# Kernel optimization log

Hardware: AMD Instinct MI355X
Metric: run time of the kernel (lower is better)

Reference implementation:

```python
import jax, jax.numpy as jnp
import numpy as np

N_NODES = 100000
N_EDGES = 800000
IN_CH = 100
HID = 100   # 2 * out_channels
OUT = 50


def setup_inputs() -> dict:
    key = jax.random.key(0)
    ks = jax.random.split(key, 6)
    x = jax.random.normal(ks[0], (N_NODES, IN_CH), dtype=jnp.float32)
    edge_index = jax.random.randint(ks[1], (2, N_EDGES), 0, N_NODES, dtype=jnp.int32)
    # Glorot-ish init for the three GCN layer weights; zero biases.
    W1 = jax.random.normal(ks[2], (IN_CH, HID), dtype=jnp.float32) * (1.0 / np.sqrt(IN_CH))
    b1 = jnp.zeros((HID,), dtype=jnp.float32)
    W_mu = jax.random.normal(ks[3], (HID, OUT), dtype=jnp.float32) * (1.0 / np.sqrt(HID))
    b_mu = jnp.zeros((OUT,), dtype=jnp.float32)
    W_ls = jax.random.normal(ks[4], (HID, OUT), dtype=jnp.float32) * (1.0 / np.sqrt(HID))
    b_ls = jnp.zeros((OUT,), dtype=jnp.float32)
    return {"x": x, "edge_index": edge_index, "W1": W1, "b1": b1,
            "W_mu": W_mu, "b_mu": b_mu, "W_ls": W_ls, "b_ls": b_ls}


def _gcn_conv(x, W, b, src, dst, deg_inv_sqrt, n):
    # GCNConv: out = D^-1/2 (A + I) D^-1/2 (x W) + b
    h = x @ W                                      # transform first (smaller messages)
    norm = deg_inv_sqrt[src] * deg_inv_sqrt[dst]   # [E]
    agg = jax.ops.segment_sum(h[src] * norm[:, None], dst, num_segments=n)
    agg = agg + h * (deg_inv_sqrt * deg_inv_sqrt)[:, None]  # self-loop term
    return agg + b


def reference(x, edge_index, W1, b1, W_mu, b_mu, W_ls, b_ls):
    n = x.shape[0]
    src, dst = edge_index[0], edge_index[1]
    # degree with self-loops (GCN normalization, edge_weight = 1)
    deg = jax.ops.segment_sum(jnp.ones((edge_index.shape[1],), jnp.float32), dst,
                              num_segments=n) + 1.0
    deg_inv_sqrt = jax.lax.rsqrt(deg)
    h = jax.nn.relu(_gcn_conv(x, W1, b1, src, dst, deg_inv_sqrt, n))
    # dropout is identity in eval mode (p applied only during training)
    mu = _gcn_conv(h, W_mu, b_mu, src, dst, deg_inv_sqrt, n)
    logstd = _gcn_conv(h, W_ls, b_ls, src, dst, deg_inv_sqrt, n)
    return mu, logstd
```

## Files before the change

kernel.cpp:

```cpp
#include <hip/hip_runtime.h>

#define NN 100000
#define NE 800000
#define NBLK 196
#define BCAP 6144
#define EPB 8192
#define NPART ((NE + EPB - 1) / EPB)
#define PACKBLK 56

typedef unsigned short ushort_t;
typedef unsigned int uint_t;
typedef __attribute__((ext_vector_type(8))) short short8;
typedef __attribute__((ext_vector_type(4))) float floatx4;

__device__ __forceinline__ float bf2f(ushort_t u) {
    union { unsigned int i; float f; } v; v.i = ((unsigned int)u) << 16; return v.f;
}
__device__ __forceinline__ ushort_t f2bf(float f) {
    union { float f; unsigned int i; } v; v.f = f;
    unsigned int b = v.i + 0x7FFF + ((v.i >> 16) & 1);
    return (ushort_t)(b >> 16);
}
__device__ __forceinline__ uint_t pack2(float a, float b) {
    return (uint_t)f2bf(a) | ((uint_t)f2bf(b) << 16);
}

__global__ __launch_bounds__(256) void k_part(const int* __restrict__ src,
                                              const int* __restrict__ dst,
                                              int* __restrict__ bcnt,
                                              int* __restrict__ bedge,
                                              const float* __restrict__ W1,
                                              const float* __restrict__ Wmu,
                                              const float* __restrict__ Wls,
                                              uint_t* __restrict__ Wt1g,
                                              uint_t* __restrict__ Wt2g) {
    __shared__ int hist[NBLK];
    __shared__ int lbase[NBLK];
    const int blk = blockIdx.x, t = threadIdx.x;

    if (blk >= NPART) {
        int lidx = (blk - NPART) * 256 + t;
        int np = lidx >> 6;
        int kp = lidx & 63;
        int mat = np / 112, n = np - mat * 112;
        int k0 = kp * 2, k1 = k0 + 1;
        float w0 = 0.0f, w1 = 0.0f;
        if (mat == 0) {
            if (n < 100) {
                if (k0 < 100) w0 = W1[k0 * 100 + n];
                if (k1 < 100) w1 = W1[k1 * 100 + n];
            }
            Wt1g[n * 64 + kp] = pack2(w0, w1);
        } else {
            if (n < 50) {
                if (k0 < 100) w0 = Wmu[k0 * 50 + n];
                if (k1 < 100) w1 = Wmu[k1 * 50 + n];
            } else if (n < 100) {
                if (k0 < 100) w0 = Wls[k0 * 50 + (n - 50)];
                if (k1 < 100) w1 = Wls[k1 * 50 + (n - 50)];
            }
            Wt2g[n * 64 + kp] = pack2(w0, w1);
        }
        return;
    }

    const int e0 = blk * EPB;
    const int e1 = (e0 + EPB < NE) ? e0 + EPB : NE;

    if (t < NBLK) hist[t] = 0;
    __syncthreads();
    for (int e = e0 + t; e < e1; e += 256)
        atomicAdd(&hist[dst[e] >> 9], 1);
    __syncthreads();
    if (t < NBLK) {
        int h = hist[t];
        lbase[t] = (h > 0) ? atomicAdd(&bcnt[t], h) : 0;
    }
    __syncthreads();
    if (t < NBLK) hist[t] = lbase[t];
    __syncthreads();
    for (int e = e0 + t; e < e1; e += 256) {
        int d = dst[e];
        int b = d >> 9;
        int pos = atomicAdd(&hist[b], 1);
        bedge[b * BCAP + pos] = src[e] | ((d & 511) << 17);
    }
}

__global__ __launch_bounds__(256) void k_build(const int* __restrict__ bcnt,
                                               const int* __restrict__ bedge,
                                               float* __restrict__ dis,
                                               int* __restrict__ off,
                                               int* __restrict__ ssrc) {
    __shared__ int eb[BCAP];
    __shared__ int hist[512];
    __shared__ int sc[2][512];
    __shared__ int red[4];
    const int b = blockIdx.x, t = threadIdx.x;
    const int cnt = bcnt[b];
    const int* be = bedge + (size_t)b * BCAP;
    const int g0 = b * 512;

    hist[t] = 0; hist[t + 256] = 0;
    int part = (t < b) ? bcnt[t] : 0;
    #pragma unroll
    for (int o = 32; o > 0; o >>= 1) part += __shfl_down(part, o, 64);
    if ((t & 63) == 0) red[t >> 6] = part;
    __syncthreads();

    for (int i = t; i < cnt; i += 256) {
        int v = be[i];
        eb[i] = v;
        atomicAdd(&hist[v >> 17], 1);
    }
    __syncthreads();
    const int base0 = red[0] + red[1] + red[2] + red[3];

    sc[0][t] = hist[t];
    sc[0][t + 256] = hist[t + 256];
    __syncthreads();
    int c = 0;
    for (int o = 1; o < 512; o <<= 1) {
        int nxt = c ^ 1;
        #pragma unroll
        for (int q = 0; q < 2; ++q) {
            int j = t + q * 256;
            sc[nxt][j] = sc[c][j] + ((j >= o) ? sc[c][j - o] : 0);
        }
        c = nxt;
        __syncthreads();
    }

    #pragma unroll
    for (int q = 0; q < 2; ++q) {
        int j = t + q * 256, g = g0 + j;
        int o = base0 + ((j > 0) ? sc[c][j - 1] : 0);
        if (g < NN) dis[g] = rsqrtf((float)hist[j] + 1.0f);
        if (g <= NN) off[g] = o;
        hist[j] = o;
    }
    __syncthreads();

    for (int i = t; i < cnt; i += 256) {
        int v = eb[i];
        int pos = atomicAdd(&hist[v >> 17], 1);
        ssrc[pos] = v & 0x1FFFF;
    }
}

__global__ __launch_bounds__(256) void k_gemm1_mfma(
    const float* __restrict__ X, const uint_t* __restrict__ Wtg,
    const float* __restrict__ dis,
    ushort_t* __restrict__ H)
{
    __shared__ ushort_t Ws[112 * 136];
    const int tid = threadIdx.x;
    const int row0 = blockIdx.x * 64;

    for (int idx = tid; idx < 112 * 16; idx += 256) {
        int n = idx >> 4, c = idx & 15;
        uint4 v = *(const uint4*)&Wtg[n * 64 + c * 4];
        *(uint4*)&Ws[n * 136 + c * 8] = v;
    }
    __syncthreads();

    const int wave = tid >> 6, lane = tid & 63;
    const int quad = lane >> 4, l16 = lane & 15;
    int row = row0 + wave * 16 + l16;
    if (row >= NN) row = NN - 1;
    const float* xp = X + (size_t)row * 100;

    floatx4 acc[7];
    #pragma unroll
    for (int t = 0; t < 7; ++t) acc[t] = (floatx4){0.f, 0.f, 0.f, 0.f};

    #pragma unroll
    for (int ks = 0; ks < 4; ++ks) {
        const int kb = ks * 32 + quad * 8;
        short8 af;
        if (ks < 3) {
            float4 u = *(const float4*)&xp[kb];
            float4 v = *(const float4*)&xp[kb + 4];
            af[0] = (short)f2bf(u.x); af[1] = (short)f2bf(u.y);
            af[2] = (short)f2bf(u.z); af[3] = (short)f2bf(u.w);
            af[4] = (short)f2bf(v.x); af[5] = (short)f2bf(v.y);
            af[6] = (short)f2bf(v.z); af[7] = (short)f2bf(v.w);
        } else {
            af = (short8){0, 0, 0, 0, 0, 0, 0, 0};
            if (quad == 0) {
                float4 u = *(const float4*)&xp[96];
                af[0] = (short)f2bf(u.x); af[1] = (short)f2bf(u.y);
                af[2] = (short)f2bf(u.z); af[3] = (short)f2bf(u.w);
            }
        }
        #pragma unroll
        for (int t = 0; t < 7; ++t) {
            short8 bf = *(const short8*)&Ws[(t * 16 + l16) * 136 + kb];
            acc[t] = __builtin_amdgcn_mfma_f32_16x16x32_bf16(af, bf, acc[t], 0, 0, 0);
        }
    }

    const int mbase = row0 + wave * 16 + quad * 4;
    #pragma unroll
    for (int reg = 0; reg < 4; ++reg) {
        int m = mbase + reg;
        if (m >= NN) continue;
        float dd = dis[m];
        #pragma unroll
        for (int t = 0; t < 7; ++t) {
            int n = t * 16 + l16;
            H[(size_t)m * 128 + n] = (n < 100) ? f2bf(acc[t][reg] * dd) : (ushort_t)0;
        }
        H[(size_t)m * 128 + 112 + l16] = 0;
    }
}

__global__ __launch_bounds__(256) void k_gemm2_mfma(
    const ushort_t* __restrict__ A,
    const uint_t* __restrict__ Wtg,
    const float* __restrict__ bmu, const float* __restrict__ bls,
    float* __restrict__ outmu, float* __restrict__ outls)
{
    __shared__ ushort_t Ws[112 * 136];
    const int tid = threadIdx.x;
    const int row0 = blockIdx.x * 64;

    for (int idx = tid; idx < 112 * 16; idx += 256) {
        int n = idx >> 4, c = idx & 15;
        uint4 v = *(const uint4*)&Wtg[n * 64 + c * 4];
        *(uint4*)&Ws[n * 136 + c * 8] = v;
    }
    __syncthreads();

    const int wave = tid >> 6, lane = tid & 63;
    const int quad = lane >> 4, l16 = lane & 15;
    int arow = row0 + wave * 16 + l16;
    if (arow >= NN) arow = NN - 1;

    floatx4 acc[7];
    #pragma unroll
    for (int t = 0; t < 7; ++t) acc[t] = (floatx4){0.f, 0.f, 0.f, 0.f};

    #pragma unroll
    for (int k0 = 0; k0 < 128; k0 += 32) {
        short8 af = *(const short8*)&A[(size_t)arow * 128 + k0 + quad * 8];
        #pragma unroll
        for (int t = 0; t < 7; ++t) {
            short8 bf = *(const short8*)&Ws[(t * 16 + l16) * 136 + k0 + quad * 8];
            acc[t] = __builtin_amdgcn_mfma_f32_16x16x32_bf16(af, bf, acc[t], 0, 0, 0);
        }
    }

    const int mbase = row0 + wave * 16 + quad * 4;
    #pragma unroll
    for (int reg = 0; reg < 4; ++reg) {
        int m = mbase + reg;
        if (m >= NN) continue;
        #pragma unroll
        for (int t = 0; t < 7; ++t) {
            int n = t * 16 + l16;
            if (n < 50) {
                outmu[(size_t)m * 50 + n] = acc[t][reg] + bmu[n];
            } else if (n < 100) {
                outls[(size_t)m * 50 + (n - 50)] = acc[t][reg] + bls[n - 50];
            }
        }
    }
}

template<int PHASE>
__global__ __launch_bounds__(256) void k_agg(
    const ushort_t* __restrict__ Hin,
    const int* __restrict__ off, const int* __restrict__ ssrc,
    const float* __restrict__ dis, const float* __restrict__ bias,
    ushort_t* __restrict__ outb)
{
    int i = blockIdx.x * 256 + threadIdx.x;
    if (i >= NN * 8) return;
    int node = i >> 3;
    int col = (i & 7) * 16;

    float a[16];
    {
        short8 u = *(const short8*)(Hin + (size_t)node * 128 + col);
        short8 v = *(const short8*)(Hin + (size_t)node * 128 + col + 8);
        #pragma unroll
        for (int j = 0; j < 8; ++j) { a[j] = bf2f((ushort_t)u[j]); a[8 + j] = bf2f((ushort_t)v[j]); }
    }

    int e0 = off[node], e1 = off[node + 1];
    int e = e0;
    for (; e + 3 < e1; e += 4) {
        int s0 = ssrc[e], s1 = ssrc[e + 1], s2 = ssrc[e + 2], s3 = ssrc[e + 3];
        short8 u0 = *(const short8*)(Hin + (size_t)s0 * 128 + col);
        short8 v0 = *(const short8*)(Hin + (size_t)s0 * 128 + col + 8);
        short8 u1 = *(const short8*)(Hin + (size_t)s1 * 128 + col);
        short8 v1 = *(const short8*)(Hin + (size_t)s1 * 128 + col + 8);
        short8 u2 = *(const short8*)(Hin + (size_t)s2 * 128 + col);
        short8 v2 = *(const short8*)(Hin + (size_t)s2 * 128 + col + 8);
        short8 u3 = *(const short8*)(Hin + (size_t)s3 * 128 + col);
        short8 v3 = *(const short8*)(Hin + (size_t)s3 * 128 + col + 8);
        #pragma unroll
        for (int j = 0; j < 8; ++j) {
            a[j]     += bf2f((ushort_t)u0[j]) + bf2f((ushort_t)u1[j])
                      + bf2f((ushort_t)u2[j]) + bf2f((ushort_t)u3[j]);
            a[8 + j] += bf2f((ushort_t)v0[j]) + bf2f((ushort_t)v1[j])
                      + bf2f((ushort_t)v2[j]) + bf2f((ushort_t)v3[j]);
        }
    }
    for (; e < e1; ++e) {
        int s0 = ssrc[e];
        short8 u0 = *(const short8*)(Hin + (size_t)s0 * 128 + col);
        short8 v0 = *(const short8*)(Hin + (size_t)s0 * 128 + col + 8);
        #pragma unroll
        for (int j = 0; j < 8; ++j) {
            a[j] += bf2f((ushort_t)u0[j]);
            a[8 + j] += bf2f((ushort_t)v0[j]);
        }
    }

    float d = dis[node];
    short8 o0, o1;
    if (PHASE == 1) {
        float b[16];
        #pragma unroll
        for (int j = 0; j < 16; ++j) {
            int cj = col + j;
            b[j] = (cj < 100) ? bias[cj] : 0.0f;
        }
        #pragma unroll
        for (int j = 0; j < 8; ++j) {
            float h0 = fmaxf(a[j] * d + b[j], 0.0f) * d;
            float h1 = fmaxf(a[8 + j] * d + b[8 + j], 0.0f) * d;
            o0[j] = (short)f2bf(h0);
            o1[j] = (short)f2bf(h1);
        }
    } else {
        #pragma unroll
        for (int j = 0; j < 8; ++j) {
            o0[j] = (short)f2bf(a[j] * d);
            o1[j] = (short)f2bf(a[8 + j] * d);
        }
    }
    *(short8*)(outb + (size_t)node * 128 + col) = o0;
    *(short8*)(outb + (size_t)node * 128 + col + 8) = o1;
}

extern "C" void kernel_launch(void* const* d_in, const int* in_sizes, int n_in,
                              void* d_out, int out_size, void* d_ws, size_t ws_size,
                              hipStream_t stream)
{
    const float* x   = (const float*)d_in[0];
    const int*   ei  = (const int*)d_in[1];
    const float* W1  = (const float*)d_in[2];
    const float* b1  = (const float*)d_in[3];
    const float* Wmu = (const float*)d_in[4];
    const float* bmu = (const float*)d_in[5];
    const float* Wls = (const float*)d_in[6];
    const float* bls = (const float*)d_in[7];
    float* out = (float*)d_out;

    const int* src = ei;
    const int* dst = ei + NE;

    int*   wsI  = (int*)d_ws;
    float* wsF  = (float*)d_ws;
    int*      off  = wsI + 100000;
    float*    dis  = wsF + 200704;
    uint_t*   Wt1g = (uint_t*)(wsI + 300704);
    uint_t*   Wt2g = (uint_t*)(wsI + 307872);
    int*      bcnt = wsI + 315040;
    int*      ssrc = wsI + 315296;
    int*      bedge= wsI + 1115296;
    ushort_t* H1b  = (ushort_t*)(wsI + 2319520);
    ushort_t* hb   = (ushort_t*)(wsI + 8719520);
    ushort_t* A2b  = (ushort_t*)(wsI + 15119520);

    hipMemsetAsync(bcnt, 0, 256 * sizeof(int), stream);
    k_part<<<NPART + PACKBLK, 256, 0, stream>>>(src, dst, bcnt, bedge,
                                                W1, Wmu, Wls, Wt1g, Wt2g);
    k_build<<<NBLK, 256, 0, stream>>>(bcnt, bedge, dis, off, ssrc);

    const int gblk = (NN + 63) / 64;
    k_gemm1_mfma<<<gblk, 256, 0, stream>>>(x, Wt1g, dis, H1b);
    k_agg<1><<<(NN * 8 + 255) / 256, 256, 0, stream>>>(H1b, off, ssrc, dis, b1, hb);
    k_agg<2><<<(NN * 8 + 255) / 256, 256, 0, stream>>>(hb, off, ssrc, dis, b1, A2b);
    k_gemm2_mfma<<<gblk, 256, 0, stream>>>(A2b, Wt2g, bmu, bls,
                                           out, out + (size_t)NN * 50);
}
```

Before: 247.2 us.

## Shrink bf16 feature row stride from 128 to 112 and deepen gather unroll

Intermediate bf16 feature matrices now use a 112-element row stride instead of 128, so each aggregation thread group covers 7 column chunks per node instead of 8. This removes 16 dead padding columns from every gathered row and cuts gather bytes and thread count. The gather loop also gets an 8-edge unrolled body with loads issued before accumulation, and launch bounds request 4 blocks per CU. The second GEMM zero-fills the last K slice for the missing columns, and rows of 224 bytes may straddle cache lines differently than 256-byte rows.

```diff
diff --git a/kernel.cpp b/kernel.cpp
--- a/kernel.cpp
+++ b/kernel.cpp
@@ -7,6 +7,7 @@
 #define EPB 8192
 #define NPART ((NE + EPB - 1) / EPB)
 #define PACKBLK 56
+#define HS 112
 
 typedef unsigned short ushort_t;
 typedef unsigned int uint_t;
@@ -209,9 +210,8 @@
         #pragma unroll
         for (int t = 0; t < 7; ++t) {
             int n = t * 16 + l16;
-            H[(size_t)m * 128 + n] = (n < 100) ? f2bf(acc[t][reg] * dd) : (ushort_t)0;
-        }
-        H[(size_t)m * 128 + 112 + l16] = 0;
+            H[(size_t)m * HS + n] = (n < 100) ? f2bf(acc[t][reg] * dd) : (ushort_t)0;
+        }
     }
 }
 
@@ -236,14 +236,22 @@
     const int quad = lane >> 4, l16 = lane & 15;
     int arow = row0 + wave * 16 + l16;
     if (arow >= NN) arow = NN - 1;
+    const ushort_t* ap = A + (size_t)arow * HS;
 
     floatx4 acc[7];
     #pragma unroll
     for (int t = 0; t < 7; ++t) acc[t] = (floatx4){0.f, 0.f, 0.f, 0.f};
 
     #pragma unroll
-    for (int k0 = 0; k0 < 128; k0 += 32) {
-        short8 af = *(const short8*)&A[(size_t)arow * 128 + k0 + quad * 8];
+    for (int ks = 0; ks < 4; ++ks) {
+        const int k0 = ks * 32;
+        short8 af;
+        if (ks < 3) {
+            af = *(const short8*)&ap[k0 + quad * 8];
+        } else {
+            if (quad < 2) af = *(const short8*)&ap[96 + quad * 8];
+            else af = (short8){0, 0, 0, 0, 0, 0, 0, 0};
+        }
         #pragma unroll
         for (int t = 0; t < 7; ++t) {
             short8 bf = *(const short8*)&Ws[(t * 16 + l16) * 136 + k0 + quad * 8];
@@ -269,49 +277,71 @@
 }
 
 template<int PHASE>
-__global__ __launch_bounds__(256) void k_agg(
+__global__ __launch_bounds__(256, 4) void k_agg(
     const ushort_t* __restrict__ Hin,
     const int* __restrict__ off, const int* __restrict__ ssrc,
     const float* __restrict__ dis, const float* __restrict__ bias,
     ushort_t* __restrict__ outb)
 {
     int i = blockIdx.x * 256 + threadIdx.x;
-    if (i >= NN * 8) return;
-    int node = i >> 3;
-    int col = (i & 7) * 16;
-
+    if (i >= NN * 7) return;
+    int node = i / 7;
+    int col = (i - node * 7) * 16;
+    const ushort_t* hbase = Hin + col;
+
+    float d = dis[node];
     float a[16];
     {
-        short8 u = *(const short8*)(Hin + (size_t)node * 128 + col);
-        short8 v = *(const short8*)(Hin + (size_t)node * 128 + col + 8);
+        short8 u = *(const short8*)(hbase + (size_t)node * HS);
+        short8 v = *(const short8*)(hbase + (size_t)node * HS + 8);
         #pragma unroll
         for (int j = 0; j < 8; ++j) { a[j] = bf2f((ushort_t)u[j]); a[8 + j] = bf2f((ushort_t)v[j]); }
     }
 
     int e0 = off[node], e1 = off[node + 1];
     int e = e0;
+    for (; e + 7 < e1; e += 8) {
+        int s[8];
+        #pragma unroll
+        for (int q = 0; q < 8; ++q) s[q] = ssrc[e + q];
+        short8 uu[8], vv[8];
+        #pragma unroll
+        for (int q = 0; q < 8; ++q) {
+            uu[q] = *(const short8*)(hbase + (size_t)s[q] * HS);
+            vv[q] = *(const short8*)(hbase + (size_t)s[q] * HS + 8);
+        }
+        #pragma unroll
+        for (int q = 0; q < 8; ++q) {
+            #pragma unroll
+            for (int j = 0; j < 8; ++j) {
+                a[j]     += bf2f((ushort_t)uu[q][j]);
+                a[8 + j] += bf2f((ushort_t)vv[q][j]);
+            }
+        }
+    }
     for (; e + 3 < e1; e += 4) {
-        int s0 = ssrc[e], s1 = ssrc[e + 1], s2 = ssrc[e + 2], s3 = ssrc[e + 3];
-        short8 u0 = *(const short8*)(Hin + (size_t)s0 * 128 + col);
-        short8 v0 = *(const short8*)(Hin + (size_t)s0 * 128 + col + 8);
-        short8 u1 = *(const short8*)(Hin + (size_t)s1 * 128 + col);
-        short8 v1 = *(const short8*)(Hin + (size_t)s1 * 128 + col + 8);
-        short8 u2 = *(const short8*)(Hin + (size_t)s2 * 128 + col);
-        short8 v2 = *(const short8*)(Hin + (size_t)s2 * 128 + col + 8);
-        short8 u3 = *(const short8*)(Hin + (size_t)s3 * 128 + col);
-        short8 v3 = *(const short8*)(Hin + (size_t)s3 * 128 + col + 8);
-        #pragma unroll
-        for (int j = 0; j < 8; ++j) {
-            a[j]     += bf2f((ushort_t)u0[j]) + bf2f((ushort_t)u1[j])
-                      + bf2f((ushort_t)u2[j]) + bf2f((ushort_t)u3[j]);
-            a[8 + j] += bf2f((ushort_t)v0[j]) + bf2f((ushort_t)v1[j])
-                      + bf2f((ushort_t)v2[j]) + bf2f((ushort_t)v3[j]);
+        int s[4];
+        #pragma unroll
+        for (int q = 0; q < 4; ++q) s[q] = ssrc[e + q];
+        short8 uu[4], vv[4];
+        #pragma unroll
+        for (int q = 0; q < 4; ++q) {
+            uu[q] = *(const short8*)(hbase + (size_t)s[q] * HS);
+            vv[q] = *(const short8*)(hbase + (size_t)s[q] * HS + 8);
+        }
+        #pragma unroll
+        for (int q = 0; q < 4; ++q) {
+            #pragma unroll
+            for (int j = 0; j < 8; ++j) {
+                a[j]     += bf2f((ushort_t)uu[q][j]);
+                a[8 + j] += bf2f((ushort_t)vv[q][j]);
+            }
         }
     }
     for (; e < e1; ++e) {
         int s0 = ssrc[e];
-        short8 u0 = *(const short8*)(Hin + (size_t)s0 * 128 + col);
-        short8 v0 = *(const short8*)(Hin + (size_t)s0 * 128 + col + 8);
+        short8 u0 = *(const short8*)(hbase + (size_t)s0 * HS);
+        short8 v0 = *(const short8*)(hbase + (size_t)s0 * HS + 8);
         #pragma unroll
         for (int j = 0; j < 8; ++j) {
             a[j] += bf2f((ushort_t)u0[j]);
@@ -319,7 +349,6 @@
         }
     }
 
-    float d = dis[node];
     short8 o0, o1;
     if (PHASE == 1) {
         float b[16];
@@ -342,8 +371,8 @@
             o1[j] = (short)f2bf(a[8 + j] * d);
         }
     }
-    *(short8*)(outb + (size_t)node * 128 + col) = o0;
-    *(short8*)(outb + (size_t)node * 128 + col + 8) = o1;
+    *(short8*)(outb + (size_t)node * HS + col) = o0;
+    *(short8*)(outb + (size_t)node * HS + col + 8) = o1;
 }
 
 extern "C" void kernel_launch(void* const* d_in, const int* in_sizes, int n_in,
@@ -375,6 +404,7 @@
     ushort_t* H1b  = (ushort_t*)(wsI + 2319520);
     ushort_t* hb   = (ushort_t*)(wsI + 8719520);
     ushort_t* A2b  = (ushort_t*)(wsI + 15119520);
+    (void)ws_size;
 
     hipMemsetAsync(bcnt, 0, 256 * sizeof(int), stream);
     k_part<<<NPART + PACKBLK, 256, 0, stream>>>(src, dst, bcnt, bedge,
@@ -382,9 +412,10 @@
     k_build<<<NBLK, 256, 0, stream>>>(bcnt, bedge, dis, off, ssrc);
 
     const int gblk = (NN + 63) / 64;
+    const int ablk = (NN * 7 + 255) / 256;
     k_gemm1_mfma<<<gblk, 256, 0, stream>>>(x, Wt1g, dis, H1b);
-    k_agg<1><<<(NN * 8 + 255) / 256, 256, 0, stream>>>(H1b, off, ssrc, dis, b1, hb);
-    k_agg<2><<<(NN * 8 + 255) / 256, 256, 0, stream>>>(hb, off, ssrc, dis, b1, A2b);
+    k_agg<1><<<ablk, 256, 0, stream>>>(H1b, off, ssrc, dis, b1, hb);
+    k_agg<2><<<ablk, 256, 0, stream>>>(hb, off, ssrc, dis, b1, A2b);
     k_gemm2_mfma<<<gblk, 256, 0, stream>>>(A2b, Wt2g, bmu, bls,
                                            out, out + (size_t)NN * 50);
 }
```

New measurement: 249.9 us. About the same (+1.1%).

## Replace bucketed two-pass CSR build with global-degree atomics and per-node placement

Applied to the files above, without the earlier changes.

The CSR construction no longer buckets edges into 512-node bins and sorts them in LDS. Degrees are now counted with global atomics per destination, a scan kernel turns them into offsets and cursors, and a placement kernel scatters each src into ssrc with a global atomicAdd on its node cursor. This drops the bedge intermediate buffer and the LDS-heavy build kernel. In exchange it relies on many contended global atomics with scattered writes, and edges within a node end up in nondeterministic order.

```diff
diff --git a/kernel.cpp b/kernel.cpp
--- a/kernel.cpp
+++ b/kernel.cpp
@@ -3,9 +3,8 @@
 #define NN 100000
 #define NE 800000
 #define NBLK 196
-#define BCAP 6144
-#define EPB 8192
-#define NPART ((NE + EPB - 1) / EPB)
+#define EPB2 2048
+#define NPART2 ((NE + EPB2 - 1) / EPB2)
 #define PACKBLK 56
 
 typedef unsigned short ushort_t;
@@ -25,21 +24,19 @@
     return (uint_t)f2bf(a) | ((uint_t)f2bf(b) << 16);
 }
 
-__global__ __launch_bounds__(256) void k_part(const int* __restrict__ src,
-                                              const int* __restrict__ dst,
-                                              int* __restrict__ bcnt,
-                                              int* __restrict__ bedge,
-                                              const float* __restrict__ W1,
-                                              const float* __restrict__ Wmu,
-                                              const float* __restrict__ Wls,
-                                              uint_t* __restrict__ Wt1g,
-                                              uint_t* __restrict__ Wt2g) {
+__global__ __launch_bounds__(256) void k_deg(const int* __restrict__ dst,
+                                             int* __restrict__ bcnt,
+                                             int* __restrict__ deg,
+                                             const float* __restrict__ W1,
+                                             const float* __restrict__ Wmu,
+                                             const float* __restrict__ Wls,
+                                             uint_t* __restrict__ Wt1g,
+                                             uint_t* __restrict__ Wt2g) {
     __shared__ int hist[NBLK];
-    __shared__ int lbase[NBLK];
     const int blk = blockIdx.x, t = threadIdx.x;
 
-    if (blk >= NPART) {
-        int lidx = (blk - NPART) * 256 + t;
+    if (blk >= NPART2) {
+        int lidx = (blk - NPART2) * 256 + t;
         int np = lidx >> 6;
         int kp = lidx & 63;
         int mat = np / 112, n = np - mat * 112;
@@ -64,61 +61,44 @@
         return;
     }
 
-    const int e0 = blk * EPB;
-    const int e1 = (e0 + EPB < NE) ? e0 + EPB : NE;
+    const int e0 = blk * EPB2;
+    const int e1 = (e0 + EPB2 < NE) ? e0 + EPB2 : NE;
 
     if (t < NBLK) hist[t] = 0;
     __syncthreads();
-    for (int e = e0 + t; e < e1; e += 256)
-        atomicAdd(&hist[dst[e] >> 9], 1);
+    for (int e = e0 + t; e < e1; e += 256) {
+        int d = dst[e];
+        atomicAdd(&deg[d], 1);
+        atomicAdd(&hist[d >> 9], 1);
+    }
     __syncthreads();
     if (t < NBLK) {
         int h = hist[t];
-        lbase[t] = (h > 0) ? atomicAdd(&bcnt[t], h) : 0;
-    }
-    __syncthreads();
-    if (t < NBLK) hist[t] = lbase[t];
-    __syncthreads();
-    for (int e = e0 + t; e < e1; e += 256) {
-        int d = dst[e];
-        int b = d >> 9;
-        int pos = atomicAdd(&hist[b], 1);
-        bedge[b * BCAP + pos] = src[e] | ((d & 511) << 17);
-    }
-}
-
-__global__ __launch_bounds__(256) void k_build(const int* __restrict__ bcnt,
-                                               const int* __restrict__ bedge,
-                                               float* __restrict__ dis,
-                                               int* __restrict__ off,
-                                               int* __restrict__ ssrc) {
-    __shared__ int eb[BCAP];
-    __shared__ int hist[512];
+        if (h > 0) atomicAdd(&bcnt[t], h);
+    }
+}
+
+__global__ __launch_bounds__(256) void k_scan(const int* __restrict__ bcnt,
+                                              const int* __restrict__ deg,
+                                              float* __restrict__ dis,
+                                              int* __restrict__ off,
+                                              int* __restrict__ cur) {
     __shared__ int sc[2][512];
     __shared__ int red[4];
     const int b = blockIdx.x, t = threadIdx.x;
-    const int cnt = bcnt[b];
-    const int* be = bedge + (size_t)b * BCAP;
     const int g0 = b * 512;
 
-    hist[t] = 0; hist[t + 256] = 0;
     int part = (t < b) ? bcnt[t] : 0;
     #pragma unroll
     for (int o = 32; o > 0; o >>= 1) part += __shfl_down(part, o, 64);
     if ((t & 63) == 0) red[t >> 6] = part;
-    __syncthreads();
-
-    for (int i = t; i < cnt; i += 256) {
-        int v = be[i];
-        eb[i] = v;
-        atomicAdd(&hist[v >> 17], 1);
-    }
-    __syncthreads();
-    const int base0 = red[0] + red[1] + red[2] + red[3];
-
-    sc[0][t] = hist[t];
-    sc[0][t + 256] = hist[t + 256];
-    __syncthreads();
+
+    int d0 = (g0 + t < NN) ? deg[g0 + t] : 0;
+    int d1 = (g0 + t + 256 < NN) ? deg[g0 + t + 256] : 0;
+    sc[0][t] = d0;
+    sc[0][t + 256] = d1;
+    __syncthreads();
+
     int c = 0;
     for (int o = 1; o < 512; o <<= 1) {
         int nxt = c ^ 1;
@@ -131,20 +111,31 @@
         __syncthreads();
     }
 
+    const int base0 = red[0] + red[1] + red[2] + red[3];
     #pragma unroll
     for (int q = 0; q < 2; ++q) {
         int j = t + q * 256, g = g0 + j;
-        int o = base0 + ((j > 0) ? sc[c][j - 1] : 0);
-        if (g < NN) dis[g] = rsqrtf((float)hist[j] + 1.0f);
-        if (g <= NN) off[g] = o;
-        hist[j] = o;
-    }
-    __syncthreads();
-
-    for (int i = t; i < cnt; i += 256) {
-        int v = eb[i];
-        int pos = atomicAdd(&hist[v >> 17], 1);
-        ssrc[pos] = v & 0x1FFFF;
+        int ov = base0 + ((j > 0) ? sc[c][j - 1] : 0);
+        if (g < NN) {
+            int dv = (q == 0) ? d0 : d1;
+            dis[g] = rsqrtf((float)dv + 1.0f);
+            off[g] = ov;
+            cur[g] = ov;
+        } else if (g == NN) {
+            off[g] = ov;
+        }
+    }
+}
+
+__global__ __launch_bounds__(256) void k_place2(const int* __restrict__ src,
+                                                const int* __restrict__ dst,
+                                                int* __restrict__ cur,
+                                                int* __restrict__ ssrc) {
+    const int stride = gridDim.x * 256;
+    for (int e = blockIdx.x * 256 + threadIdx.x; e < NE; e += stride) {
+        int d = dst[e];
+        int pos = atomicAdd(&cur[d], 1);
+        ssrc[pos] = src[e];
     }
 }
 
@@ -365,26 +356,30 @@
 
     int*   wsI  = (int*)d_ws;
     float* wsF  = (float*)d_ws;
-    int*      off  = wsI + 100000;
-    float*    dis  = wsF + 200704;
-    uint_t*   Wt1g = (uint_t*)(wsI + 300704);
-    uint_t*   Wt2g = (uint_t*)(wsI + 307872);
-    int*      bcnt = wsI + 315040;
-    int*      ssrc = wsI + 315296;
-    int*      bedge= wsI + 1115296;
-    ushort_t* H1b  = (ushort_t*)(wsI + 2319520);
-    ushort_t* hb   = (ushort_t*)(wsI + 8719520);
-    ushort_t* A2b  = (ushort_t*)(wsI + 15119520);
-
-    hipMemsetAsync(bcnt, 0, 256 * sizeof(int), stream);
-    k_part<<<NPART + PACKBLK, 256, 0, stream>>>(src, dst, bcnt, bedge,
+    int*      bcnt = wsI;
+    int*      deg  = wsI + 256;
+    int*      off  = wsI + 100256;
+    int*      cur  = wsI + 200320;
+    float*    dis  = wsF + 300320;
+    uint_t*   Wt1g = (uint_t*)(wsI + 400320);
+    uint_t*   Wt2g = (uint_t*)(wsI + 407488);
+    int*      ssrc = wsI + 414656;
+    ushort_t* H1b  = (ushort_t*)(wsI + 1214656);
+    ushort_t* hb   = (ushort_t*)(wsI + 7614656);
+    ushort_t* A2b  = (ushort_t*)(wsI + 14014656);
+    (void)ws_size;
+
+    hipMemsetAsync(wsI, 0, (256 + NN) * sizeof(int), stream);
+    k_deg<<<NPART2 + PACKBLK, 256, 0, stream>>>(dst, bcnt, deg,
                                                 W1, Wmu, Wls, Wt1g, Wt2g);
-    k_build<<<NBLK, 256, 0, stream>>>(bcnt, bedge, dis, off, ssrc);
+    k_scan<<<NBLK, 256, 0, stream>>>(bcnt, deg, dis, off, cur);
+    k_place2<<<1024, 256, 0, stream>>>(src, dst, cur, ssrc);
 
     const int gblk = (NN + 63) / 64;
+    const int ablk = (NN * 8 + 255) / 256;
     k_gemm1_mfma<<<gblk, 256, 0, stream>>>(x, Wt1g, dis, H1b);
-    k_agg<1><<<(NN * 8 + 255) / 256, 256, 0, stream>>>(H1b, off, ssrc, dis, b1, hb);
-    k_agg<2><<<(NN * 8 + 255) / 256, 256, 0, stream>>>(hb, off, ssrc, dis, b1, A2b);
+    k_agg<1><<<ablk, 256, 0, stream>>>(H1b, off, ssrc, dis, b1, hb);
+    k_agg<2><<<ablk, 256, 0, stream>>>(hb, off, ssrc, dis, b1, A2b);
     k_gemm2_mfma<<<gblk, 256, 0, stream>>>(A2b, Wt2g, bmu, bls,
                                            out, out + (size_t)NN * 50);
 }
```

New measurement: 314.0 us. +27.0%, slower.

## Fuse second aggregation with output GEMM through shared memory tile

Applied to the files above, without the earlier changes.

Merges the phase-2 neighbor aggregation and the second MFMA GEMM into one kernel. Each block aggregates 64 nodes into a shared-memory bf16 tile, then runs the GEMM straight from LDS. This drops the A2b intermediate write and re-read and removes one launch. In exchange, each thread now handles 32 columns with fewer threads per node, which lowers gather parallelism and raises register pressure and LDS use per block, so occupancy may fall.

```diff
diff --git a/kernel.cpp b/kernel.cpp
--- a/kernel.cpp
+++ b/kernel.cpp
@@ -215,61 +215,7 @@
     }
 }
 
-__global__ __launch_bounds__(256) void k_gemm2_mfma(
-    const ushort_t* __restrict__ A,
-    const uint_t* __restrict__ Wtg,
-    const float* __restrict__ bmu, const float* __restrict__ bls,
-    float* __restrict__ outmu, float* __restrict__ outls)
-{
-    __shared__ ushort_t Ws[112 * 136];
-    const int tid = threadIdx.x;
-    const int row0 = blockIdx.x * 64;
-
-    for (int idx = tid; idx < 112 * 16; idx += 256) {
-        int n = idx >> 4, c = idx & 15;
-        uint4 v = *(const uint4*)&Wtg[n * 64 + c * 4];
-        *(uint4*)&Ws[n * 136 + c * 8] = v;
-    }
-    __syncthreads();
-
-    const int wave = tid >> 6, lane = tid & 63;
-    const int quad = lane >> 4, l16 = lane & 15;
-    int arow = row0 + wave * 16 + l16;
-    if (arow >= NN) arow = NN - 1;
-
-    floatx4 acc[7];
-    #pragma unroll
-    for (int t = 0; t < 7; ++t) acc[t] = (floatx4){0.f, 0.f, 0.f, 0.f};
-
-    #pragma unroll
-    for (int k0 = 0; k0 < 128; k0 += 32) {
-        short8 af = *(const short8*)&A[(size_t)arow * 128 + k0 + quad * 8];
-        #pragma unroll
-        for (int t = 0; t < 7; ++t) {
-            short8 bf = *(const short8*)&Ws[(t * 16 + l16) * 136 + k0 + quad * 8];
-            acc[t] = __builtin_amdgcn_mfma_f32_16x16x32_bf16(af, bf, acc[t], 0, 0, 0);
-        }
-    }
-
-    const int mbase = row0 + wave * 16 + quad * 4;
-    #pragma unroll
-    for (int reg = 0; reg < 4; ++reg) {
-        int m = mbase + reg;
-        if (m >= NN) continue;
-        #pragma unroll
-        for (int t = 0; t < 7; ++t) {
-            int n = t * 16 + l16;
-            if (n < 50) {
-                outmu[(size_t)m * 50 + n] = acc[t][reg] + bmu[n];
-            } else if (n < 100) {
-                outls[(size_t)m * 50 + (n - 50)] = acc[t][reg] + bls[n - 50];
-            }
-        }
-    }
-}
-
-template<int PHASE>
-__global__ __launch_bounds__(256) void k_agg(
+__global__ __launch_bounds__(256) void k_agg1(
     const ushort_t* __restrict__ Hin,
     const int* __restrict__ off, const int* __restrict__ ssrc,
     const float* __restrict__ dis, const float* __restrict__ bias,
@@ -321,29 +267,132 @@
 
     float d = dis[node];
     short8 o0, o1;
-    if (PHASE == 1) {
-        float b[16];
-        #pragma unroll
-        for (int j = 0; j < 16; ++j) {
-            int cj = col + j;
-            b[j] = (cj < 100) ? bias[cj] : 0.0f;
-        }
-        #pragma unroll
-        for (int j = 0; j < 8; ++j) {
-            float h0 = fmaxf(a[j] * d + b[j], 0.0f) * d;
-            float h1 = fmaxf(a[8 + j] * d + b[8 + j], 0.0f) * d;
-            o0[j] = (short)f2bf(h0);
-            o1[j] = (short)f2bf(h1);
-        }
-    } else {
-        #pragma unroll
-        for (int j = 0; j < 8; ++j) {
-            o0[j] = (short)f2bf(a[j] * d);
-            o1[j] = (short)f2bf(a[8 + j] * d);
-        }
+    float b[16];
+    #pragma unroll
+    for (int j = 0; j < 16; ++j) {
+        int cj = col + j;
+        b[j] = (cj < 100) ? bias[cj] : 0.0f;
+    }
+    #pragma unroll
+    for (int j = 0; j < 8; ++j) {
+        float h0 = fmaxf(a[j] * d + b[j], 0.0f) * d;
+        float h1 = fmaxf(a[8 + j] * d + b[8 + j], 0.0f) * d;
+        o0[j] = (short)f2bf(h0);
+        o1[j] = (short)f2bf(h1);
     }
     *(short8*)(outb + (size_t)node * 128 + col) = o0;
     *(short8*)(outb + (size_t)node * 128 + col + 8) = o1;
+}
+
+__global__ __launch_bounds__(256) void k_fuse2(
+    const ushort_t* __restrict__ Hin,
+    const int* __restrict__ off, const int* __restrict__ ssrc,
+    const float* __restrict__ dis,
+    const uint_t* __restrict__ Wtg,
+    const float* __restrict__ bmu, const float* __restrict__ bls,
+    float* __restrict__ outmu, float* __restrict__ outls)
+{
+    __shared__ ushort_t Ws[112 * 136];
+    __shared__ ushort_t As[64][136];
+    const int tid = threadIdx.x;
+    const int row0 = blockIdx.x * 64;
+
+    for (int idx = tid; idx < 112 * 16; idx += 256) {
+        int n = idx >> 4, c = idx & 15;
+        uint4 v = *(const uint4*)&Wtg[n * 64 + c * 4];
+        *(uint4*)&Ws[n * 136 + c * 8] = v;
+    }
+
+    {
+        const int lr = tid >> 2;
+        const int part = tid & 3;
+        const int c0 = part * 32;
+        int nd = row0 + lr;
+        if (nd >= NN) nd = NN - 1;
+        const ushort_t* selfp = Hin + (size_t)nd * 128 + c0;
+
+        float a[32];
+        #pragma unroll
+        for (int g = 0; g < 4; ++g) {
+            short8 u = *(const short8*)(selfp + g * 8);
+            #pragma unroll
+            for (int j = 0; j < 8; ++j) a[g * 8 + j] = bf2f((ushort_t)u[j]);
+        }
+
+        const int e0v = off[nd], e1v = off[nd + 1];
+        int e = e0v;
+        for (; e + 1 < e1v; e += 2) {
+            int s0 = ssrc[e], s1 = ssrc[e + 1];
+            const ushort_t* p0 = Hin + (size_t)s0 * 128 + c0;
+            const ushort_t* p1 = Hin + (size_t)s1 * 128 + c0;
+            short8 u[4], v[4];
+            #pragma unroll
+            for (int g = 0; g < 4; ++g) {
+                u[g] = *(const short8*)(p0 + g * 8);
+                v[g] = *(const short8*)(p1 + g * 8);
+            }
+            #pragma unroll
+            for (int g = 0; g < 4; ++g) {
+                #pragma unroll
+                for (int j = 0; j < 8; ++j)
+                    a[g * 8 + j] += bf2f((ushort_t)u[g][j]) + bf2f((ushort_t)v[g][j]);
+            }
+        }
+        for (; e < e1v; ++e) {
+            int s0 = ssrc[e];
+            const ushort_t* p0 = Hin + (size_t)s0 * 128 + c0;
+            #pragma unroll
+            for (int g = 0; g < 4; ++g) {
+                short8 u = *(const short8*)(p0 + g * 8);
+                #pragma unroll
+                for (int j = 0; j < 8; ++j) a[g * 8 + j] += bf2f((ushort_t)u[j]);
+            }
+        }
+
+        const float d = dis[nd];
+        #pragma unroll
+        for (int g = 0; g < 4; ++g) {
+            short8 o;
+            #pragma unroll
+            for (int j = 0; j < 8; ++j) o[j] = (short)f2bf(a[g * 8 + j] * d);
+            *(short8*)&As[lr][c0 + g * 8] = o;
+        }
+    }
+    __syncthreads();
+
+    const int wave = tid >> 6, lane = tid & 63;
+    const int quad = lane >> 4, l16 = lane & 15;
+    const int lrow = wave * 16 + l16;
+
+    floatx4 acc[7];
+    #pragma unroll
+    for (int t = 0; t < 7; ++t) acc[t] = (floatx4){0.f, 0.f, 0.f, 0.f};
+
+    #pragma unroll
+    for (int k0 = 0; k0 < 128; k0 += 32) {
+        short8 af = *(const short8*)&As[lrow][k0 + quad * 8];
+        #pragma unroll
+        for (int t = 0; t < 7; ++t) {
+            short8 bf = *(const short8*)&Ws[(t * 16 + l16) * 136 + k0 + quad * 8];
+            acc[t] = __builtin_amdgcn_mfma_f32_16x16x32_bf16(af, bf, acc[t], 0, 0, 0);
+        }
+    }
+
+    const int mbase = row0 + wave * 16 + quad * 4;
+    #pragma unroll
+    for (int reg = 0; reg < 4; ++reg) {
+        int m = mbase + reg;
+        if (m >= NN) continue;
+        #pragma unroll
+        for (int t = 0; t < 7; ++t) {
+            int n = t * 16 + l16;
+            if (n < 50) {
+                outmu[(size_t)m * 50 + n] = acc[t][reg] + bmu[n];
+            } else if (n < 100) {
+                outls[(size_t)m * 50 + (n - 50)] = acc[t][reg] + bls[n - 50];
+            }
+        }
+    }
 }
 
 extern "C" void kernel_launch(void* const* d_in, const int* in_sizes, int n_in,
@@ -374,7 +423,7 @@
     int*      bedge= wsI + 1115296;
     ushort_t* H1b  = (ushort_t*)(wsI + 2319520);
     ushort_t* hb   = (ushort_t*)(wsI + 8719520);
-    ushort_t* A2b  = (ushort_t*)(wsI + 15119520);
+    (void)ws_size;
 
     hipMemsetAsync(bcnt, 0, 256 * sizeof(int), stream);
     k_part<<<NPART + PACKBLK, 256, 0, stream>>>(src, dst, bcnt, bedge,
@@ -382,9 +431,9 @@
     k_build<<<NBLK, 256, 0, stream>>>(bcnt, bedge, dis, off, ssrc);
 
     const int gblk = (NN + 63) / 64;
+    const int ablk = (NN * 8 + 255) / 256;
     k_gemm1_mfma<<<gblk, 256, 0, stream>>>(x, Wt1g, dis, H1b);
-    k_agg<1><<<(NN * 8 + 255) / 256, 256, 0, stream>>>(H1b, off, ssrc, dis, b1, hb);
-    k_agg<2><<<(NN * 8 + 255) / 256, 256, 0, stream>>>(hb, off, ssrc, dis, b1, A2b);
-    k_gemm2_mfma<<<gblk, 256, 0, stream>>>(A2b, Wt2g, bmu, bls,
-                                           out, out + (size_t)NN * 50);
-}
+    k_agg1<<<ablk, 256, 0, stream>>>(H1b, off, ssrc, dis, b1, hb);
+    k_fuse2<<<gblk, 256, 0, stream>>>(hb, off, ssrc, dis, Wt2g, bmu, bls,
+                                      out, out + (size_t)NN * 50);
+}
```

Measured after the change: 246.7 us. About the same (-0.2%).
